# Performance work log

Measured on AMD Instinct MI355X. Metric: run time of the kernel, lower is better.

The kernel has to match this reference:

```python
import jax, jax.numpy as jnp
import numpy as np
import math

MEMORY_SLOTS = 256
NUM_PAIRS = 128
VOCAB = 32000
HIDDEN = 512
B, L = 32, 4096


def setup_inputs() -> dict:
    key = jax.random.key(0)
    ks = jax.random.split(key, 16)
    s = 0.02
    return {
        "seq": jax.random.randint(ks[0], (B, L), 0, VOCAB, dtype=jnp.int32),
        "embed": jax.random.normal(ks[1], (VOCAB, HIDDEN), jnp.float32) * s,
        "w1": jax.random.normal(ks[2], (HIDDEN, HIDDEN), jnp.float32) * s,
        "b1": jnp.zeros((HIDDEN,), jnp.float32),
        "w2": jax.random.normal(ks[3], (HIDDEN, HIDDEN), jnp.float32) * s,
        "b2": jnp.zeros((HIDDEN,), jnp.float32),
        "wg": jax.random.normal(ks[4], (HIDDEN, 1), jnp.float32) * s,
        "bg": jnp.zeros((1,), jnp.float32),
        "wq": jax.random.normal(ks[5], (HIDDEN, HIDDEN), jnp.float32) * s,
        "bq": jnp.zeros((HIDDEN,), jnp.float32),
        "wk": jax.random.normal(ks[6], (HIDDEN, HIDDEN), jnp.float32) * s,
        "bk": jnp.zeros((HIDDEN,), jnp.float32),
        "wo": jax.random.normal(ks[7], (HIDDEN, VOCAB), jnp.float32) * s,
        "bo": jnp.zeros((VOCAB,), jnp.float32),
    }


def reference(seq, embed, w1, b1, w2, b2, wg, bg, wq, bq, wk, bk, wo, bo):
    K = min(NUM_PAIRS, MEMORY_SLOTS)
    # Encoder: embedding gather + 2-layer ReLU MLP -> hidden [B, L, H]
    h = embed[seq]
    h = jax.nn.relu(h @ w1 + b1)
    h = jax.nn.relu(h @ w2 + b2)
    # Write gate: sigmoid(Linear(H->1)) -> gate_scores [B, L]
    gate_scores = jax.nn.sigmoid(jnp.squeeze(h @ wg + bg, -1))
    # Gumbel-perturbed top-k over sequence positions
    u = jax.random.uniform(jax.random.key(42), gate_scores.shape,
                           minval=1e-10, maxval=1.0)
    gumbel = -jnp.log(-jnp.log(u))
    perturbed = gate_scores + 0.1 * gumbel
    topk_vals, topk_idx = jax.lax.top_k(perturbed, K)  # [B, K]
    soft_w = jax.nn.softmax(topk_vals, axis=-1)        # [B, K]
    topk_v = jnp.take_along_axis(h, topk_idx[..., None], axis=1)  # [B, K, H]
    # Scatter weighted vectors into first K memory slots (vectorized)
    Bn, _, H = h.shape
    memory = jnp.zeros((Bn, MEMORY_SLOTS, H), h.dtype)
    memory = memory.at[:, :K, :].set(topk_v * soft_w[..., None])
    # Read head: attention of query (second-to-last token) over memory
    query = h[:, -2, :]                 # [B, H]
    q = query @ wq + bq                 # [B, H]
    k = memory @ wk + bk                # [B, S, H]
    scale = math.sqrt(float(H))
    w = jax.nn.softmax(jnp.einsum("bh,bsh->bs", q, k) / scale, axis=-1)
    read_vec = jnp.einsum("bs,bsh->bh", w, memory)
    logits = read_vec @ wo + bo         # [B, V]
    return logits, gate_scores, h
```

## Files before the change

### kernel.cpp

```cpp
#include <hip/hip_runtime.h>
#include <hip/hip_bf16.h>

#define HID    512
#define NB     32
#define SEQLEN 4096
#define NROWS  (NB * SEQLEN)
#define VOCAB_ 32000
#define KTOP   128
#define SLOTS  256
#define BM     64

typedef unsigned short ushort_t;
typedef short short8v __attribute__((ext_vector_type(8)));
typedef float f32x4 __attribute__((ext_vector_type(4)));

__device__ __forceinline__ unsigned pkbf(float lo, float hi) {
  return ((__float_as_uint(lo) + 0x8000u) >> 16) |
         ((__float_as_uint(hi) + 0x8000u) & 0xFFFF0000u);
}

__device__ __forceinline__ unsigned rotl32(unsigned x, int d) {
  return (x << d) | (x >> (32 - d));
}
__device__ __forceinline__ void threefry_0_42(unsigned& x0, unsigned& x1) {
  const unsigned k0 = 0u, k1 = 42u;
  const unsigned k2 = k0 ^ k1 ^ 0x1BD11BDAu;
  x0 += k0; x1 += k1;
#define TFR(r) { x0 += x1; x1 = rotl32(x1, r); x1 ^= x0; }
  TFR(13) TFR(15) TFR(26) TFR(6)
  x0 += k1; x1 += k2 + 1u;
  TFR(17) TFR(29) TFR(16) TFR(24)
  x0 += k2; x1 += k0 + 2u;
  TFR(13) TFR(15) TFR(26) TFR(6)
  x0 += k0; x1 += k1 + 3u;
  TFR(17) TFR(29) TFR(16) TFR(24)
  x0 += k1; x1 += k2 + 4u;
  TFR(13) TFR(15) TFR(26) TFR(6)
  x0 += k2; x1 += k0 + 5u;
#undef TFR
}
__device__ __forceinline__ float gumbel_for(size_t gid) {
  unsigned j = (unsigned)(gid & 65535u);
  unsigned x0 = j, x1 = j + 65536u;
  threefry_0_42(x0, x1);
  unsigned bits = (gid < 65536) ? x0 : x1;
  unsigned mb = (bits >> 9) | 0x3F800000u;
  float u = __uint_as_float(mb) - 1.0f;
  u = u + 1e-10f;
  u = fmaxf(u, 1e-10f);
  return -logf(-logf(u));
}

template <int NTHR, int NROWS_C>
__device__ __forceinline__ void expand_rows(
    const int* __restrict__ seq, const float* __restrict__ h_table,
    const float* __restrict__ gate_table, float* __restrict__ h_out,
    float* __restrict__ gate_out, size_t pos0, int t, int* toks)
{
  for (int i = t; i < NROWS_C; i += NTHR) toks[i] = seq[pos0 + i];
  __syncthreads();
  const int total = NROWS_C * 128;
#pragma unroll
  for (int p = t; p < total; p += NTHR) {
    int pr = p >> 7, c = p & 127;
    float4 v = *reinterpret_cast<const float4*>(
        h_table + (size_t)toks[pr] * HID + c * 4);
    *reinterpret_cast<float4*>(h_out + (pos0 + pr) * HID + c * 4) = v;
  }
  for (int i = t; i < NROWS_C; i += NTHR)
    gate_out[pos0 + i] = gate_table[toks[i]];
}

__global__ __launch_bounds__(256) void pack_weights(
    const float* __restrict__ w1, const float* __restrict__ w2,
    const float* __restrict__ wk, const float* __restrict__ embed,
    ushort_t* __restrict__ w1p, ushort_t* __restrict__ w2p,
    float* __restrict__ wkT, ushort_t* __restrict__ embd_bf, int do_embed)
{
  if (blockIdx.x < 256) {
    int gid = blockIdx.x * 256 + threadIdx.x;
    int mat = gid >> 15;
    int r   = gid & 32767;
    int kc  = r >> 11;
    int c   = (r >> 2) & 511;
    int ksub = r & 3;
    const float* src = mat ? w2 : w1;
    ushort_t*    dst = mat ? w2p : w1p;
    int k0 = kc * 32 + ksub * 8;
    unsigned pk[4];
#pragma unroll
    for (int i = 0; i < 4; ++i)
      pk[i] = pkbf(src[(size_t)(k0 + 2 * i) * HID + c],
                   src[(size_t)(k0 + 2 * i + 1) * HID + c]);
    *reinterpret_cast<uint4*>(dst + ((size_t)(kc * 512 + c) * 32 + ksub * 8)) =
        make_uint4(pk[0], pk[1], pk[2], pk[3]);
  } else if (blockIdx.x < 512) {
    int idx = (blockIdx.x - 256) * 256 + threadIdx.x;
#pragma unroll
    for (int i = 0; i < 4; ++i) {
      int e = idx + i * 65536;
      int j = e >> 9, c = e & 511;
      wkT[e] = wk[(size_t)c * HID + j];
    }
  } else if (do_embed) {
    int idx = (blockIdx.x - 512) * 256 + threadIdx.x;
#pragma unroll
    for (int i = 0; i < 4; ++i) {
      size_t e8 = (size_t)idx + (size_t)i * 524288;
      if (e8 < (size_t)VOCAB_ * HID / 8) {
        const float* s = embed + e8 * 8;
        float4 f0 = *reinterpret_cast<const float4*>(s);
        float4 f1 = *reinterpret_cast<const float4*>(s + 4);
        *reinterpret_cast<uint4*>(embd_bf + e8 * 8) =
            make_uint4(pkbf(f0.x, f0.y), pkbf(f0.z, f0.w),
                       pkbf(f1.x, f1.y), pkbf(f1.z, f1.w));
      }
    }
  }
}

__device__ __forceinline__ short8v ldsA(const char* lb, int row, int kc, int lq) {
  int byteoff = row * 1024 + ((kc * 64 + lq * 16) ^ ((row & 7) << 4));
  return *reinterpret_cast<const short8v*>(lb + byteoff);
}
__device__ __forceinline__ short8v ldB(const ushort_t* wp, int kc, int col, int lq) {
  return *reinterpret_cast<const short8v*>(wp + ((size_t)(kc * 512 + col) * 32 + lq * 8));
}

__global__ __launch_bounds__(512, 4) void mlp_table(
    const float* __restrict__ embed,
    const ushort_t* __restrict__ w1p, const float* __restrict__ b1,
    const ushort_t* __restrict__ w2p, const float* __restrict__ b2,
    const float* __restrict__ wg, const float* __restrict__ bg,
    float* __restrict__ h_table, float* __restrict__ gate_table)
{
  __shared__ ushort_t As[BM * HID];
  __shared__ float gred[8][BM];
  char* lb = (char*)As;

  const int t = threadIdx.x;
  const int wave = t >> 6, l = t & 63;
  const int lq = l >> 4, lr = l & 15;
  const size_t row0 = (size_t)blockIdx.x * BM;

  {
    int r  = t >> 3;
    int cc = t & 7;
    int swz = (r & 7) << 4;
    const float* srow = embed + (row0 + r) * HID;
#pragma unroll
    for (int ch = 0; ch < 8; ++ch) {
      int dstByte = ch * 128 + cc * 16;
      int srcByte = dstByte ^ swz;
      int e0 = srcByte >> 1;
      float4 f0 = *reinterpret_cast<const float4*>(srow + e0);
      float4 f1 = *reinterpret_cast<const float4*>(srow + e0 + 4);
      *reinterpret_cast<uint4*>(lb + r * 1024 + dstByte) =
          make_uint4(pkbf(f0.x, f0.y), pkbf(f0.z, f0.w),
                     pkbf(f1.x, f1.y), pkbf(f1.z, f1.w));
    }
  }
  __syncthreads();

  const int col0 = wave * 64;
  f32x4 acc[4][4];

#pragma unroll
  for (int fh = 0; fh < 4; ++fh)
#pragma unroll
    for (int fs = 0; fs < 4; ++fs) acc[fh][fs] = (f32x4){0.f, 0.f, 0.f, 0.f};
  {
    short8v wF[4], wN[4], aJ[4];
#pragma unroll
    for (int fh = 0; fh < 4; ++fh) wF[fh] = ldB(w1p, 0, col0 + fh * 16 + lr, lq);
#pragma unroll
    for (int kc = 0; kc < 16; ++kc) {
      if (kc < 15) {
#pragma unroll
        for (int fh = 0; fh < 4; ++fh) wN[fh] = ldB(w1p, kc + 1, col0 + fh * 16 + lr, lq);
      }
#pragma unroll
      for (int fs = 0; fs < 4; ++fs) aJ[fs] = ldsA(lb, fs * 16 + lr, kc, lq);
      __builtin_amdgcn_s_setprio(1);
#pragma unroll
      for (int fh = 0; fh < 4; ++fh)
#pragma unroll
        for (int fs = 0; fs < 4; ++fs)
          acc[fh][fs] = __builtin_amdgcn_mfma_f32_16x16x32_bf16(
              wF[fh], aJ[fs], acc[fh][fs], 0, 0, 0);
      __builtin_amdgcn_s_setprio(0);
#pragma unroll
      for (int fh = 0; fh < 4; ++fh) wF[fh] = wN[fh];
    }
  }

  {
    float4 b1v[4];
#pragma unroll
    for (int fh = 0; fh < 4; ++fh)
      b1v[fh] = *reinterpret_cast<const float4*>(b1 + col0 + fh * 16 + lq * 4);
    __syncthreads();
#pragma unroll
    for (int fh = 0; fh < 4; ++fh)
#pragma unroll
      for (int fs = 0; fs < 4; ++fs) {
        f32x4 a = acc[fh][fs];
        float v0 = fmaxf(a[0] + b1v[fh].x, 0.f);
        float v1 = fmaxf(a[1] + b1v[fh].y, 0.f);
        float v2 = fmaxf(a[2] + b1v[fh].z, 0.f);
        float v3 = fmaxf(a[3] + b1v[fh].w, 0.f);
        int row = fs * 16 + lr;
        int off = row * 1024 + ((col0 * 2 + fh * 32 + lq * 8) ^ ((row & 7) << 4));
        *reinterpret_cast<uint2*>(lb + off) = make_uint2(pkbf(v0, v1), pkbf(v2, v3));
      }
    __syncthreads();
  }

#pragma unroll
  for (int fh = 0; fh < 4; ++fh)
#pragma unroll
    for (int fs = 0; fs < 4; ++fs) acc[fh][fs] = (f32x4){0.f, 0.f, 0.f, 0.f};
  {
    short8v wF[4], wN[4], aJ[4];
#pragma unroll
    for (int fh = 0; fh < 4; ++fh) wF[fh] = ldB(w2p, 0, col0 + fh * 16 + lr, lq);
#pragma unroll
    for (int kc = 0; kc < 16; ++kc) {
      if (kc < 15) {
#pragma unroll
        for (int fh = 0; fh < 4; ++fh) wN[fh] = ldB(w2p, kc + 1, col0 + fh * 16 + lr, lq);
      }
#pragma unroll
      for (int fs = 0; fs < 4; ++fs) aJ[fs] = ldsA(lb, fs * 16 + lr, kc, lq);
      __builtin_amdgcn_s_setprio(1);
#pragma unroll
      for (int fh = 0; fh < 4; ++fh)
#pragma unroll
        for (int fs = 0; fs < 4; ++fs)
          acc[fh][fs] = __builtin_amdgcn_mfma_f32_16x16x32_bf16(
              wF[fh], aJ[fs], acc[fh][fs], 0, 0, 0);
      __builtin_amdgcn_s_setprio(0);
#pragma unroll
      for (int fh = 0; fh < 4; ++fh) wF[fh] = wN[fh];
    }
  }

  {
    float4 b2v[4], wgv[4];
#pragma unroll
    for (int fh = 0; fh < 4; ++fh) {
      b2v[fh] = *reinterpret_cast<const float4*>(b2 + col0 + fh * 16 + lq * 4);
      wgv[fh] = *reinterpret_cast<const float4*>(wg + col0 + fh * 16 + lq * 4);
    }
    float ps[4] = {0.f, 0.f, 0.f, 0.f};
    __syncthreads();
#pragma unroll
    for (int half = 0; half < 2; ++half) {
#pragma unroll
      for (int fh = 0; fh < 4; ++fh)
#pragma unroll
        for (int fs2 = 0; fs2 < 2; ++fs2) {
          int fs = half * 2 + fs2;
          f32x4 a = acc[fh][fs];
          float v0 = fmaxf(a[0] + b2v[fh].x, 0.f);
          float v1 = fmaxf(a[1] + b2v[fh].y, 0.f);
          float v2 = fmaxf(a[2] + b2v[fh].z, 0.f);
          float v3 = fmaxf(a[3] + b2v[fh].w, 0.f);
          int lrow = fs2 * 16 + lr;
          int cb = (col0 + fh * 16 + lq * 4) * 4;
          *reinterpret_cast<float4*>(lb + lrow * 2048 + (cb ^ (lr << 4))) =
              make_float4(v0, v1, v2, v3);
          ps[fs] += v0 * wgv[fh].x + v1 * wgv[fh].y + v2 * wgv[fh].z + v3 * wgv[fh].w;
        }
      __syncthreads();
#pragma unroll
      for (int j = 0; j < 8; ++j) {
        int p = j * 512 + t;
        int row = p >> 7, c16 = p & 127;
        float4 v = *reinterpret_cast<const float4*>(
            lb + row * 2048 + ((c16 * 16) ^ ((row & 15) << 4)));
        *reinterpret_cast<float4*>(
            h_table + (row0 + half * 32 + row) * HID + c16 * 4) = v;
      }
      __syncthreads();
    }
#pragma unroll
    for (int fs = 0; fs < 4; ++fs) {
      ps[fs] += __shfl_xor(ps[fs], 16);
      ps[fs] += __shfl_xor(ps[fs], 32);
    }
    if (l < 16) {
#pragma unroll
      for (int fs = 0; fs < 4; ++fs) gred[wave][fs * 16 + lr] = ps[fs];
    }
  }
  __syncthreads();
  if (t < BM) {
    float x = bg[0];
#pragma unroll
    for (int w = 0; w < 8; ++w) x += gred[w][t];
    gate_table[row0 + t] = 1.f / (1.f + expf(-x));
  }
}

__global__ __launch_bounds__(512, 4) void mlp_mfma(
    const int* __restrict__ seq, const float* __restrict__ embed,
    const ushort_t* __restrict__ embd_bf, int use_glds,
    const ushort_t* __restrict__ w1p, const float* __restrict__ b1,
    const ushort_t* __restrict__ w2p, const float* __restrict__ b2,
    const float* __restrict__ wg, const float* __restrict__ bg,
    float* __restrict__ h_out, float* __restrict__ gate_out,
    float* __restrict__ pert_out)
{
  __shared__ ushort_t As[BM * HID];
  __shared__ float gred[8][BM];
  char* lb = (char*)As;

  const int t = threadIdx.x;
  const int wave = t >> 6, l = t & 63;
  const int lq = l >> 4, lr = l & 15;
  const size_t row0 = (size_t)blockIdx.x * BM;

  if (use_glds) {
#pragma unroll
    for (int i = 0; i < 8; ++i) {
      int r = wave * 8 + i;
      int tok = seq[row0 + r];
      int swz = (r & 7) << 4;
      const ushort_t* src = embd_bf + (size_t)tok * HID + (((l * 16) ^ swz) >> 1);
      __builtin_amdgcn_global_load_lds(
          (const __attribute__((address_space(1))) void*)src,
          (__attribute__((address_space(3))) void*)(As + r * 512), 16, 0, 0);
    }
  } else {
    int r  = t >> 3;
    int cc = t & 7;
    int swz = (r & 7) << 4;
    int tok = seq[row0 + r];
    const float* srow = embed + (size_t)tok * HID;
#pragma unroll
    for (int ch = 0; ch < 8; ++ch) {
      int dstByte = ch * 128 + cc * 16;
      int srcByte = dstByte ^ swz;
      int e0 = srcByte >> 1;
      float4 f0 = *reinterpret_cast<const float4*>(srow + e0);
      float4 f1 = *reinterpret_cast<const float4*>(srow + e0 + 4);
      *reinterpret_cast<uint4*>(lb + r * 1024 + dstByte) =
          make_uint4(pkbf(f0.x, f0.y), pkbf(f0.z, f0.w),
                     pkbf(f1.x, f1.y), pkbf(f1.z, f1.w));
    }
  }
  __syncthreads();

  const int col0 = wave * 64;
  f32x4 acc[4][4];

#pragma unroll
  for (int fh = 0; fh < 4; ++fh)
#pragma unroll
    for (int fs = 0; fs < 4; ++fs) acc[fh][fs] = (f32x4){0.f, 0.f, 0.f, 0.f};
  {
    short8v wF[4], wN[4], aJ[4];
#pragma unroll
    for (int fh = 0; fh < 4; ++fh) wF[fh] = ldB(w1p, 0, col0 + fh * 16 + lr, lq);
#pragma unroll
    for (int kc = 0; kc < 16; ++kc) {
      if (kc < 15) {
#pragma unroll
        for (int fh = 0; fh < 4; ++fh) wN[fh] = ldB(w1p, kc + 1, col0 + fh * 16 + lr, lq);
      }
#pragma unroll
      for (int fs = 0; fs < 4; ++fs) aJ[fs] = ldsA(lb, fs * 16 + lr, kc, lq);
      __builtin_amdgcn_s_setprio(1);
#pragma unroll
      for (int fh = 0; fh < 4; ++fh)
#pragma unroll
        for (int fs = 0; fs < 4; ++fs)
          acc[fh][fs] = __builtin_amdgcn_mfma_f32_16x16x32_bf16(
              wF[fh], aJ[fs], acc[fh][fs], 0, 0, 0);
      __builtin_amdgcn_s_setprio(0);
#pragma unroll
      for (int fh = 0; fh < 4; ++fh) wF[fh] = wN[fh];
    }
  }
  {
    float4 b1v[4];
#pragma unroll
    for (int fh = 0; fh < 4; ++fh)
      b1v[fh] = *reinterpret_cast<const float4*>(b1 + col0 + fh * 16 + lq * 4);
    __syncthreads();
#pragma unroll
    for (int fh = 0; fh < 4; ++fh)
#pragma unroll
      for (int fs = 0; fs < 4; ++fs) {
        f32x4 a = acc[fh][fs];
        float v0 = fmaxf(a[0] + b1v[fh].x, 0.f);
        float v1 = fmaxf(a[1] + b1v[fh].y, 0.f);
        float v2 = fmaxf(a[2] + b1v[fh].z, 0.f);
        float v3 = fmaxf(a[3] + b1v[fh].w, 0.f);
        int row = fs * 16 + lr;
        int off = row * 1024 + ((col0 * 2 + fh * 32 + lq * 8) ^ ((row & 7) << 4));
        *reinterpret_cast<uint2*>(lb + off) = make_uint2(pkbf(v0, v1), pkbf(v2, v3));
      }
    __syncthreads();
  }
#pragma unroll
  for (int fh = 0; fh < 4; ++fh)
#pragma unroll
    for (int fs = 0; fs < 4; ++fs) acc[fh][fs] = (f32x4){0.f, 0.f, 0.f, 0.f};
  {
    short8v wF[4], wN[4], aJ[4];
#pragma unroll
    for (int fh = 0; fh < 4; ++fh) wF[fh] = ldB(w2p, 0, col0 + fh * 16 + lr, lq);
#pragma unroll
    for (int kc = 0; kc < 16; ++kc) {
      if (kc < 15) {
#pragma unroll
        for (int fh = 0; fh < 4; ++fh) wN[fh] = ldB(w2p, kc + 1, col0 + fh * 16 + lr, lq);
      }
#pragma unroll
      for (int fs = 0; fs < 4; ++fs) aJ[fs] = ldsA(lb, fs * 16 + lr, kc, lq);
      __builtin_amdgcn_s_setprio(1);
#pragma unroll
      for (int fh = 0; fh < 4; ++fh)
#pragma unroll
        for (int fs = 0; fs < 4; ++fs)
          acc[fh][fs] = __builtin_amdgcn_mfma_f32_16x16x32_bf16(
              wF[fh], aJ[fs], acc[fh][fs], 0, 0, 0);
      __builtin_amdgcn_s_setprio(0);
#pragma unroll
      for (int fh = 0; fh < 4; ++fh) wF[fh] = wN[fh];
    }
  }
  {
    float4 b2v[4], wgv[4];
#pragma unroll
    for (int fh = 0; fh < 4; ++fh) {
      b2v[fh] = *reinterpret_cast<const float4*>(b2 + col0 + fh * 16 + lq * 4);
      wgv[fh] = *reinterpret_cast<const float4*>(wg + col0 + fh * 16 + lq * 4);
    }
    float ps[4] = {0.f, 0.f, 0.f, 0.f};
    __syncthreads();
#pragma unroll
    for (int half = 0; half < 2; ++half) {
#pragma unroll
      for (int fh = 0; fh < 4; ++fh)
#pragma unroll
        for (int fs2 = 0; fs2 < 2; ++fs2) {
          int fs = half * 2 + fs2;
          f32x4 a = acc[fh][fs];
          float v0 = fmaxf(a[0] + b2v[fh].x, 0.f);
          float v1 = fmaxf(a[1] + b2v[fh].y, 0.f);
          float v2 = fmaxf(a[2] + b2v[fh].z, 0.f);
          float v3 = fmaxf(a[3] + b2v[fh].w, 0.f);
          int lrow = fs2 * 16 + lr;
          int cb = (col0 + fh * 16 + lq * 4) * 4;
          *reinterpret_cast<float4*>(lb + lrow * 2048 + (cb ^ (lr << 4))) =
              make_float4(v0, v1, v2, v3);
          ps[fs] += v0 * wgv[fh].x + v1 * wgv[fh].y + v2 * wgv[fh].z + v3 * wgv[fh].w;
        }
      __syncthreads();
#pragma unroll
      for (int j = 0; j < 8; ++j) {
        int p = j * 512 + t;
        int row = p >> 7, c16 = p & 127;
        float4 v = *reinterpret_cast<const float4*>(
            lb + row * 2048 + ((c16 * 16) ^ ((row & 15) << 4)));
        *reinterpret_cast<float4*>(
            h_out + (row0 + half * 32 + row) * HID + c16 * 4) = v;
      }
      __syncthreads();
    }
#pragma unroll
    for (int fs = 0; fs < 4; ++fs) {
      ps[fs] += __shfl_xor(ps[fs], 16);
      ps[fs] += __shfl_xor(ps[fs], 32);
    }
    if (l < 16) {
#pragma unroll
      for (int fs = 0; fs < 4; ++fs) gred[wave][fs * 16 + lr] = ps[fs];
    }
  }
  __syncthreads();
  if (t < BM) {
    float x = bg[0];
#pragma unroll
    for (int w = 0; w < 8; ++w) x += gred[w][t];
    float gate = 1.f / (1.f + expf(-x));
    size_t gid = row0 + t;
    gate_out[gid] = gate;
    pert_out[gid] = gate + 0.1f * gumbel_for(gid);
  }
}

__global__ __launch_bounds__(1024) void prep_ex(
    const float* __restrict__ pert, const int* __restrict__ seq,
    const float* __restrict__ gate_table, int tmode,
    int* __restrict__ tidx, float* __restrict__ sw,
    const float* __restrict__ hsrc,
    const float* __restrict__ wq, const float* __restrict__ bq,
    const float* __restrict__ wkT, const float* __restrict__ bk,
    float* __restrict__ tv_all, float* __restrict__ qbk_all,
    float* __restrict__ h_out, float* __restrict__ gate_out)
{
  const int t = threadIdx.x;
  if (blockIdx.x >= 2 * NB) {
    __shared__ int toks[128];
    size_t pos0 = (size_t)(blockIdx.x - 2 * NB) * 128;
    expand_rows<1024, 128>(seq, hsrc, gate_table, h_out, gate_out, pos0, t, toks);
    return;
  }
  if (blockIdx.x < NB) {
    __shared__ unsigned hist[16][256];
    __shared__ unsigned hsum[256];
    __shared__ unsigned sPfx, sNeed;
    __shared__ int wtot[16], wbase[16];
    __shared__ float ovals[KTOP];
    __shared__ int   oidx[KTOP];
    __shared__ float smax, ssum;
    const int b = blockIdx.x;
    const int wid = t >> 6, lane = t & 63;

    unsigned key[4]; float val[4];
    if (tmode) {
      int4 s4 = *reinterpret_cast<const int4*>(seq + (size_t)b * SEQLEN + t * 4);
      size_t gid0 = (size_t)b * SEQLEN + t * 4;
      val[0] = gate_table[s4.x] + 0.1f * gumbel_for(gid0 + 0);
      val[1] = gate_table[s4.y] + 0.1f * gumbel_for(gid0 + 1);
      val[2] = gate_table[s4.z] + 0.1f * gumbel_for(gid0 + 2);
      val[3] = gate_table[s4.w] + 0.1f * gumbel_for(gid0 + 3);
    } else {
      float4 vv = *reinterpret_cast<const float4*>(pert + (size_t)b * SEQLEN + t * 4);
      val[0] = vv.x; val[1] = vv.y; val[2] = vv.z; val[3] = vv.w;
    }
#pragma unroll
    for (int i = 0; i < 4; ++i) {
      unsigned u = __float_as_uint(val[i]);
      key[i] = (u & 0x80000000u) ? ~u : (u | 0x80000000u);
    }
    if (t == 0) { sPfx = 0u; sNeed = KTOP; }

    unsigned mask = 0u;
    for (int shift = 24; shift >= 0; shift -= 8) {
      for (int i = t; i < 16 * 256; i += 1024) ((unsigned*)hist)[i] = 0u;
      __syncthreads();
      unsigned pfx = sPfx;
#pragma unroll
      for (int i = 0; i < 4; ++i)
        if ((key[i] & mask) == pfx)
          atomicAdd(&hist[wid][(key[i] >> shift) & 0xFFu], 1u);
      __syncthreads();
      if (t < 256) {
        unsigned s = 0;
#pragma unroll
        for (int w = 0; w < 16; ++w) s += hist[w][t];
        hsum[t] = s;
      }
      __syncthreads();
      if (t == 0) {
        unsigned need = sNeed, cum = 0; int v = 255;
        for (; v > 0; --v) {
          unsigned c = hsum[v];
          if (cum + c >= need) break;
          cum += c;
        }
        sPfx = sPfx | ((unsigned)v << shift);
        sNeed = need - cum;
      }
      mask |= 0xFFu << shift;
      __syncthreads();
    }
    const unsigned T = sPfx;
    const int needEq = (int)sNeed;
    const int cntGT = KTOP - needEq;

    int cGT = 0, cEQ = 0;
#pragma unroll
    for (int i = 0; i < 4; ++i) {
      if (key[i] > T) cGT++;
      else if (key[i] == T) cEQ++;
    }
    int comb = cGT | (cEQ << 16);
    int inc = comb;
    for (int off = 1; off < 64; off <<= 1) {
      int n = __shfl_up(inc, off);
      if (lane >= off) inc += n;
    }
    if (lane == 63) wtot[wid] = inc;
    __syncthreads();
    if (t == 0) {
      int r = 0;
      for (int w = 0; w < 16; ++w) { wbase[w] = r; r += wtot[w]; }
    }
    __syncthreads();
    int ex = wbase[wid] + inc - comb;
    int posGT = ex & 0xFFFF;
    int posEQ = ex >> 16;
#pragma unroll
    for (int i = 0; i < 4; ++i) {
      if (key[i] > T) {
        oidx[posGT] = t * 4 + i; ovals[posGT] = val[i]; posGT++;
      } else if (key[i] == T) {
        if (posEQ < needEq) { oidx[cntGT + posEQ] = t * 4 + i; ovals[cntGT + posEQ] = val[i]; }
        posEQ++;
      }
    }
    __syncthreads();
    if (t == 0) {
      float m = -1e30f;
      for (int i = 0; i < KTOP; ++i) m = fmaxf(m, ovals[i]);
      float s = 0.f;
      for (int i = 0; i < KTOP; ++i) s += expf(ovals[i] - m);
      smax = m; ssum = s;
    }
    __syncthreads();
    if (t < KTOP) {
      tidx[b * KTOP + t] = oidx[t];
      sw[b * KTOP + t] = expf(ovals[t] - smax) / ssum;
    }
  } else {
    __shared__ float hq[HID], qv[HID];
    __shared__ float part[1024];
    __shared__ float red[8];
    const int b = blockIdx.x - NB;
    const int c = t & 511, half = t >> 9;

    if (t < HID) {
      size_t row = tmode ? (size_t)seq[(size_t)b * SEQLEN + (SEQLEN - 2)]
                         : (size_t)b * SEQLEN + (SEQLEN - 2);
      hq[t] = hsrc[row * HID + t];
    }
    __syncthreads();
    {
      float acc = 0.f;
      const int k0 = half * 256;
      for (int k = k0; k < k0 + 256; k += 4) {
        float4 a = *reinterpret_cast<const float4*>(&hq[k]);
        acc = fmaf(a.x, wq[(size_t)(k + 0) * HID + c], acc);
        acc = fmaf(a.y, wq[(size_t)(k + 1) * HID + c], acc);
        acc = fmaf(a.z, wq[(size_t)(k + 2) * HID + c], acc);
        acc = fmaf(a.w, wq[(size_t)(k + 3) * HID + c], acc);
      }
      part[t] = acc;
    }
    __syncthreads();
    if (t < HID) qv[t] = part[t] + part[t + 512] + bq[t];
    __syncthreads();
    {
      float acc = 0.f;
      const int k0 = half * 256;
      for (int k = k0; k < k0 + 256; k += 4) {
        float4 a = *reinterpret_cast<const float4*>(&qv[k]);
        acc = fmaf(a.x, wkT[(size_t)(k + 0) * HID + c], acc);
        acc = fmaf(a.y, wkT[(size_t)(k + 1) * HID + c], acc);
        acc = fmaf(a.z, wkT[(size_t)(k + 2) * HID + c], acc);
        acc = fmaf(a.w, wkT[(size_t)(k + 3) * HID + c], acc);
      }
      part[t] = acc;
    }
    __syncthreads();
    if (t < HID) tv_all[(size_t)b * HID + t] = part[t] + part[t + 512];
    float pb = (t < HID) ? qv[t] * bk[t] : 0.f;
    for (int o = 32; o > 0; o >>= 1) pb += __shfl_down(pb, o);
    if ((t & 63) == 0 && t < HID) red[t >> 6] = pb;
    __syncthreads();
    if (t == 0) {
      float s = 0.f;
      for (int i = 0; i < 8; ++i) s += red[i];
      qbk_all[b] = s;
    }
  }
}

__global__ __launch_bounds__(512) void attn_ex(
    const int* __restrict__ seq, const float* __restrict__ gate_table, int tmode,
    const float* __restrict__ hsrc, const int* __restrict__ tidx,
    const float* __restrict__ sw, const float* __restrict__ tv_all,
    const float* __restrict__ qbk_all, float* __restrict__ rv_out,
    float* __restrict__ h_out, float* __restrict__ gate_out, size_t e_row0)
{
  const int t = threadIdx.x;
  if (blockIdx.x >= NB) {
    __shared__ int toks[64];
    size_t pos0 = e_row0 + (size_t)(blockIdx.x - NB) * 64;
    expand_rows<512, 64>(seq, hsrc, gate_table, h_out, gate_out, pos0, t, toks);
    return;
  }
  __shared__ float tv[HID];
  __shared__ float sc[SLOTS], cs[KTOP], ssw[KTOP];
  __shared__ int   sidx[KTOP];
  const int b = blockIdx.x;
  const int wave = t >> 6, lane = t & 63;
  if (t < KTOP) {
    int idx = tidx[b * KTOP + t];
    sidx[t] = tmode ? seq[(size_t)b * SEQLEN + idx] : (b * SEQLEN + idx);
    ssw[t] = sw[b * KTOP + t];
  }
  tv[t] = tv_all[(size_t)b * HID + t];
  const float qbk_s = qbk_all[b];
  __syncthreads();
  const float rscale = 0.044194173824159216f;
  for (int ss = 0; ss < 16; ++ss) {
    int s = wave * 16 + ss;
    const float* hr = hsrc + (size_t)sidx[s] * HID;
    float4 a0 = *reinterpret_cast<const float4*>(hr + lane * 8);
    float4 a1 = *reinterpret_cast<const float4*>(hr + lane * 8 + 4);
    float4 t0 = *reinterpret_cast<const float4*>(&tv[lane * 8]);
    float4 t1 = *reinterpret_cast<const float4*>(&tv[lane * 8 + 4]);
    float pv = a0.x * t0.x + a0.y * t0.y + a0.z * t0.z + a0.w * t0.w
             + a1.x * t1.x + a1.y * t1.y + a1.z * t1.z + a1.w * t1.w;
    for (int o = 32; o > 0; o >>= 1) pv += __shfl_down(pv, o);
    if (lane == 0) sc[s] = fmaf(ssw[s], pv, qbk_s) * rscale;
  }
  if (t >= KTOP && t < SLOTS) sc[t] = qbk_s * rscale;
  __syncthreads();
  if (wave == 0) {
    float v0 = sc[lane], v1 = sc[lane + 64], v2 = sc[lane + 128], v3 = sc[lane + 192];
    float m = fmaxf(fmaxf(v0, v1), fmaxf(v2, v3));
    for (int o = 32; o > 0; o >>= 1) m = fmaxf(m, __shfl_xor(m, o));
    float e0 = expf(v0 - m), e1 = expf(v1 - m), e2 = expf(v2 - m), e3 = expf(v3 - m);
    float s = e0 + e1 + e2 + e3;
    for (int o = 32; o > 0; o >>= 1) s += __shfl_xor(s, o);
    float inv = 1.f / s;
    sc[lane] = e0 * inv; sc[lane + 64] = e1 * inv;
    sc[lane + 128] = e2 * inv; sc[lane + 192] = e3 * inv;
  }
  __syncthreads();
  if (t < KTOP) cs[t] = sc[t] * ssw[t];
  __syncthreads();
  float r = 0.f;
  for (int s = 0; s < KTOP; ++s)
    r = fmaf(cs[s], hsrc[(size_t)sidx[s] * HID + t], r);
  rv_out[(size_t)b * HID + t] = r;
}

__global__ __launch_bounds__(256) void logits_ex(
    const float* __restrict__ rv, const float* __restrict__ wo,
    const float* __restrict__ bo, float* __restrict__ out,
    const int* __restrict__ seq, const float* __restrict__ hsrc,
    const float* __restrict__ gate_table,
    float* __restrict__ h_out, float* __restrict__ gate_out, size_t e_row0)
{
  const int t = threadIdx.x;
  if (blockIdx.x >= 1000) {
    __shared__ int toks[32];
    size_t pos0 = e_row0 + (size_t)(blockIdx.x - 1000) * 32;
    expand_rows<256, 32>(seq, hsrc, gate_table, h_out, gate_out, pos0, t, toks);
    return;
  }
  __shared__ float part[8][32][NB + 1];
  const int c  = t & 31;
  const int kq = t >> 5;
  const int v  = blockIdx.x * 32 + c;
  float acc[NB];
#pragma unroll
  for (int b = 0; b < NB; ++b) acc[b] = 0.f;
  const int k0 = kq * 64;
  for (int k = k0; k < k0 + 64; k += 4) {
    float q0 = wo[(size_t)(k + 0) * VOCAB_ + v];
    float q1 = wo[(size_t)(k + 1) * VOCAB_ + v];
    float q2 = wo[(size_t)(k + 2) * VOCAB_ + v];
    float q3 = wo[(size_t)(k + 3) * VOCAB_ + v];
#pragma unroll
    for (int b = 0; b < NB; ++b) {
      float4 rb = *reinterpret_cast<const float4*>(rv + b * HID + k);
      acc[b] = fmaf(rb.x, q0, acc[b]);
      acc[b] = fmaf(rb.y, q1, acc[b]);
      acc[b] = fmaf(rb.z, q2, acc[b]);
      acc[b] = fmaf(rb.w, q3, acc[b]);
    }
  }
#pragma unroll
  for (int b = 0; b < NB; ++b) part[kq][c][b] = acc[b];
  __syncthreads();
  for (int i = t; i < 32 * NB; i += 256) {
    int cc = i & 31, b = i >> 5;
    float s = part[0][cc][b] + part[1][cc][b] + part[2][cc][b] + part[3][cc][b]
            + part[4][cc][b] + part[5][cc][b] + part[6][cc][b] + part[7][cc][b]
            + bo[blockIdx.x * 32 + cc];
    out[(size_t)b * VOCAB_ + blockIdx.x * 32 + cc] = s;
  }
}

extern "C" void kernel_launch(void* const* d_in, const int* in_sizes, int n_in,
                              void* d_out, int out_size, void* d_ws, size_t ws_size,
                              hipStream_t stream) {
  const int*   seq   = (const int*)d_in[0];
  const float* embed = (const float*)d_in[1];
  const float* w1 = (const float*)d_in[2];
  const float* b1 = (const float*)d_in[3];
  const float* w2 = (const float*)d_in[4];
  const float* b2 = (const float*)d_in[5];
  const float* wg = (const float*)d_in[6];
  const float* bg = (const float*)d_in[7];
  const float* wq = (const float*)d_in[8];
  const float* bq = (const float*)d_in[9];
  const float* wk = (const float*)d_in[10];
  const float* bk = (const float*)d_in[11];
  const float* wo = (const float*)d_in[12];
  const float* bo = (const float*)d_in[13];

  float* logits = (float*)d_out;
  float* gate   = logits + (size_t)NB * VOCAB_;
  float* hmat   = gate + NROWS;

  float* ws   = (float*)d_ws;
  float* pert = ws;
  int*   tidx = (int*)(ws + 131072);
  float* sw   = ws + 135168;
  float* rv   = ws + 139264;
  ushort_t* w1p = (ushort_t*)(ws + 155648);
  ushort_t* w2p = w1p + (size_t)HID * HID;
  float* wkT    = ws + 417792;
  float* tv_all = ws + 679936;
  float* qbk_all = ws + 696320;
  float* gate_table = ws + 696384;
  float* h_table = ws + 728384;
  ushort_t* embd_bf = (ushort_t*)(ws + 696384);

  const size_t need_table = ((size_t)728384 + (size_t)VOCAB_ * HID) * 4;
  const size_t need_glds  = ((size_t)696384 + (size_t)VOCAB_ * HID / 2) * 4;
  const int use_table = (ws_size >= need_table) ? 1 : 0;
  const int use_glds  = (!use_table && ws_size >= need_glds) ? 1 : 0;

  hipLaunchKernelGGL(pack_weights, dim3(use_glds ? 2560 : 512), dim3(256), 0, stream,
                     w1, w2, wk, embed, w1p, w2p, wkT, embd_bf, use_glds);
  if (use_table) {
    hipLaunchKernelGGL(mlp_table, dim3(VOCAB_ / BM), dim3(512), 0, stream,
                       embed, w1p, b1, w2p, b2, wg, bg, h_table, gate_table);
    hipLaunchKernelGGL(prep_ex, dim3(2 * NB + 512), dim3(1024), 0, stream,
                       (const float*)nullptr, seq, gate_table, 1, tidx, sw,
                       h_table, wq, bq, wkT, bk, tv_all, qbk_all, hmat, gate);
    hipLaunchKernelGGL(attn_ex, dim3(NB + 256), dim3(512), 0, stream,
                       seq, gate_table, 1, h_table, tidx, sw, tv_all, qbk_all,
                       rv, hmat, gate, (size_t)65536);
    hipLaunchKernelGGL(logits_ex, dim3(1000 + 1536), dim3(256), 0, stream,
                       rv, wo, bo, logits, seq, h_table, gate_table,
                       hmat, gate, (size_t)81920);
  } else {
    hipLaunchKernelGGL(mlp_mfma, dim3(NROWS / BM), dim3(512), 0, stream,
                       seq, embed, embd_bf, use_glds,
                       w1p, b1, w2p, b2, wg, bg, hmat, gate, pert);
    hipLaunchKernelGGL(prep_ex, dim3(2 * NB), dim3(1024), 0, stream,
                       pert, seq, (const float*)nullptr, 0, tidx, sw,
                       hmat, wq, bq, wkT, bk, tv_all, qbk_all, hmat, gate);
    hipLaunchKernelGGL(attn_ex, dim3(NB), dim3(512), 0, stream,
                       seq, (const float*)nullptr, 0, hmat, tidx, sw, tv_all,
                       qbk_all, rv, hmat, gate, (size_t)0);
    hipLaunchKernelGGL(logits_ex, dim3(1000), dim3(256), 0, stream,
                       rv, wo, bo, logits, seq, hmat, (const float*)nullptr,
                       hmat, gate, (size_t)0);
  }
}
```

Measured before the change: 255.9 us.

## Parallelize radix-select bucket search and softmax reductions, rebalance expand-row split

The serial single-thread scan over the 256-bin histogram in each radix pass becomes a parallel suffix-sum scan across 256 threads, and the serial max/sum softmax over the top-k values becomes a warp-shuffle reduction. This shortens the critical path of the top-k blocks, which otherwise hold up the fused prep kernel. The row-expansion work is also shifted so fewer expand blocks run alongside prep and more run alongside attention. The scan adds several extra __syncthreads per radix pass.

```diff
diff --git a/kernel.cpp b/kernel.cpp
--- a/kernel.cpp
+++ b/kernel.cpp
@@ -513,10 +513,13 @@
   if (blockIdx.x < NB) {
     __shared__ unsigned hist[16][256];
     __shared__ unsigned hsum[256];
+    __shared__ unsigned sscan[256];
     __shared__ unsigned sPfx, sNeed;
     __shared__ int wtot[16], wbase[16];
     __shared__ float ovals[KTOP];
     __shared__ int   oidx[KTOP];
+    __shared__ float es[KTOP];
+    __shared__ float red2[2];
     __shared__ float smax, ssum;
     const int b = blockIdx.x;
     const int wid = t >> 6, lane = t & 63;
@@ -555,17 +558,23 @@
 #pragma unroll
         for (int w = 0; w < 16; ++w) s += hist[w][t];
         hsum[t] = s;
+        sscan[t] = s;
       }
       __syncthreads();
-      if (t == 0) {
-        unsigned need = sNeed, cum = 0; int v = 255;
-        for (; v > 0; --v) {
-          unsigned c = hsum[v];
-          if (cum + c >= need) break;
-          cum += c;
+#pragma unroll
+      for (int off = 1; off < 256; off <<= 1) {
+        unsigned add = 0;
+        if (t < 256 && t + off < 256) add = sscan[t + off];
+        __syncthreads();
+        if (t < 256) sscan[t] += add;
+        __syncthreads();
+      }
+      {
+        unsigned need = sNeed;
+        if (t < 256 && sscan[t] >= need && (t == 255 || sscan[t + 1] < need)) {
+          sPfx = sPfx | ((unsigned)t << shift);
+          sNeed = need - (sscan[t] - hsum[t]);
         }
-        sPfx = sPfx | ((unsigned)v << shift);
-        sNeed = need - cum;
       }
       mask |= 0xFFu << shift;
       __syncthreads();
@@ -606,17 +615,28 @@
       }
     }
     __syncthreads();
-    if (t == 0) {
-      float m = -1e30f;
-      for (int i = 0; i < KTOP; ++i) m = fmaxf(m, ovals[i]);
-      float s = 0.f;
-      for (int i = 0; i < KTOP; ++i) s += expf(ovals[i] - m);
-      smax = m; ssum = s;
-    }
+    if (t < KTOP) {
+      float m = ovals[t];
+#pragma unroll
+      for (int o = 32; o > 0; o >>= 1) m = fmaxf(m, __shfl_xor(m, o));
+      if (lane == 0) red2[wid] = m;
+    }
+    __syncthreads();
+    if (t == 0) smax = fmaxf(red2[0], red2[1]);
+    __syncthreads();
+    if (t < KTOP) {
+      float e = expf(ovals[t] - smax);
+      es[t] = e;
+#pragma unroll
+      for (int o = 32; o > 0; o >>= 1) e += __shfl_xor(e, o);
+      if (lane == 0) red2[wid] = e;
+    }
+    __syncthreads();
+    if (t == 0) ssum = red2[0] + red2[1];
     __syncthreads();
     if (t < KTOP) {
       tidx[b * KTOP + t] = oidx[t];
-      sw[b * KTOP + t] = expf(ovals[t] - smax) / ssum;
+      sw[b * KTOP + t] = es[t] / ssum;
     }
   } else {
     __shared__ float hq[HID], qv[HID];
@@ -828,12 +848,12 @@
   if (use_table) {
     hipLaunchKernelGGL(mlp_table, dim3(VOCAB_ / BM), dim3(512), 0, stream,
                        embed, w1p, b1, w2p, b2, wg, bg, h_table, gate_table);
-    hipLaunchKernelGGL(prep_ex, dim3(2 * NB + 512), dim3(1024), 0, stream,
+    hipLaunchKernelGGL(prep_ex, dim3(2 * NB + 384), dim3(1024), 0, stream,
                        (const float*)nullptr, seq, gate_table, 1, tidx, sw,
                        h_table, wq, bq, wkT, bk, tv_all, qbk_all, hmat, gate);
-    hipLaunchKernelGGL(attn_ex, dim3(NB + 256), dim3(512), 0, stream,
+    hipLaunchKernelGGL(attn_ex, dim3(NB + 512), dim3(512), 0, stream,
                        seq, gate_table, 1, h_table, tidx, sw, tv_all, qbk_all,
-                       rv, hmat, gate, (size_t)65536);
+                       rv, hmat, gate, (size_t)49152);
     hipLaunchKernelGGL(logits_ex, dim3(1000 + 1536), dim3(256), 0, stream,
                        rv, wo, bo, logits, seq, h_table, gate_table,
                        hmat, gate, (size_t)81920);
```

After: 259.0 us. No clear change (+1.2%).
